# Performance work log

Measured on AMD Instinct MI355X. Metric: run time of the kernel, lower is better.

Reference implementation:

```python
import jax, jax.numpy as jnp
import numpy as np

N_NODES = 100000
N_EDGES = 3200000
IN_CH, HID, OUT_CH = 602, 16, 41


def setup_inputs() -> dict:
    key = jax.random.key(0)
    ks = jax.random.split(key, 5)
    x = jax.random.normal(ks[0], (N_NODES, IN_CH), dtype=jnp.float32)
    edge_index = jax.random.randint(ks[1], (2, N_EDGES), 0, N_NODES, dtype=jnp.int32)
    # glorot init for weights, zeros for biases (matches reset_parameters)
    W1 = jax.random.normal(ks[2], (IN_CH, HID), dtype=jnp.float32) * np.sqrt(2.0 / (IN_CH + HID))
    b1 = jnp.zeros((HID,), dtype=jnp.float32)
    W2 = jax.random.normal(ks[3], (HID, OUT_CH), dtype=jnp.float32) * np.sqrt(2.0 / (HID + OUT_CH))
    b2 = jnp.zeros((OUT_CH,), dtype=jnp.float32)
    return {"x": x, "edge_index": edge_index, "W1": W1, "b1": b1, "W2": W2, "b2": b2}


def _sage_conv(x, src, dst, W, b, n_nodes):
    # linear transform first (16-wide), then gather-scatter-mean over edges
    h = x @ W                                   # [N, out]
    msg = h[src]                                # [E, out] gather of source nodes
    agg = jax.ops.segment_sum(msg, dst, num_segments=n_nodes)          # [N, out]
    cnt = jax.ops.segment_sum(jnp.ones((src.shape[0], 1), h.dtype), dst,
                              num_segments=n_nodes)                     # [N, 1]
    mean = agg / jnp.maximum(cnt, 1.0)          # scatter-mean (0 for isolated nodes)
    return mean + b


def reference(x, edge_index, W1, b1, W2, b2):
    src, dst = edge_index[0], edge_index[1]     # source_to_target flow
    n = x.shape[0]
    h = jax.nn.relu(_sage_conv(x, src, dst, W1, b1, n))
    # F.dropout(training=False) -> identity (inference mode)
    out = _sage_conv(h, src, dst, W2, b2, n)
    return jax.nn.log_softmax(out, axis=1)
```

## Files before the change

kernel.cpp:

```cpp
#include <hip/hip_runtime.h>
#include <hip/hip_fp16.h>
#include <cmath>

#define NN 100000
#define NE 3200000
#define CIN 602
#define CH 16
#define COUT 41
#define KTL 32

#define NPB 128
#define NB  ((NN + NPB - 1) / NPB)
#define EPC 32
#define ECHUNK (256 * EPC)
#define EB  ((NE + ECHUNK - 1) / ECHUNK)

__device__ __half g_h1h[NN * CH];
__device__ __half g_h1bh[NN * CH];
__device__ int   g_rs[NN + 1];
__device__ int   g_csr[NE];
__device__ int2  g_pair[NE];
__device__ int   g_cnt[NB * EB];
__device__ int   g_colsum[NB];
__device__ int   g_bbase[NB + 1];

__device__ __forceinline__ int clamp_node(int v) {
    return v < 0 ? 0 : (v >= NN ? NN - 1 : v);
}

__global__ __launch_bounds__(256) void fallback_zero_out_k(float* __restrict__ out, int n) {
    int i = blockIdx.x * blockDim.x + threadIdx.x;
    if (i < n) out[i] = 0.0f;
}

__global__ __launch_bounds__(256) void count_k(const int* __restrict__ ei) {
    __shared__ int h[NB];
    const int t = threadIdx.x;
    for (int i = t; i < NB; i += 256) h[i] = 0;
    __syncthreads();
    const int base = blockIdx.x * ECHUNK;
#pragma unroll
    for (int j = 0; j < EPC; ++j) {
        int e = base + j * 256 + t;
        if (e < NE) {
            int d = clamp_node(ei[NE + e]);
            atomicAdd(&h[d >> 7], 1);
        }
    }
    __syncthreads();
    for (int i = t; i < NB; i += 256) g_cnt[i * EB + blockIdx.x] = h[i];
}

__global__ __launch_bounds__(256) void scanA_k() {
    const int b = blockIdx.x;
    const int t = threadIdx.x;
    __shared__ int a[512];
    __shared__ int sh[256];
    a[t]       = (t < EB)       ? g_cnt[b * EB + t]       : 0;
    a[t + 256] = (t + 256 < EB) ? g_cnt[b * EB + t + 256] : 0;
    __syncthreads();
    int e0 = a[2 * t], e1 = a[2 * t + 1];
    int sum = e0 + e1;
    sh[t] = sum;
    __syncthreads();
    for (int off = 1; off < 256; off <<= 1) {
        int v = (t >= off) ? sh[t - off] : 0;
        __syncthreads();
        sh[t] += v;
        __syncthreads();
    }
    int run = sh[t] - sum;
    if (2 * t < EB)     g_cnt[b * EB + 2 * t]     = run;
    if (2 * t + 1 < EB) g_cnt[b * EB + 2 * t + 1] = run + e0;
    if (t == 255) g_colsum[b] = sh[255];
}

__global__ __launch_bounds__(1024) void scanB_k() {
    const int t = threadIdx.x;
    __shared__ int sh[1024];
    int v = (t < NB) ? g_colsum[t] : 0;
    sh[t] = v;
    __syncthreads();
    for (int off = 1; off < 1024; off <<= 1) {
        int u = (t >= off) ? sh[t - off] : 0;
        __syncthreads();
        sh[t] += u;
        __syncthreads();
    }
    if (t < NB) g_bbase[t] = sh[t] - v;
    if (t == 1023) {
        g_bbase[NB] = sh[1023];
        g_rs[NN]    = sh[1023];
    }
}

__global__ __launch_bounds__(256) void scatter_k(const int* __restrict__ ei) {
    __shared__ int lb[NB];
    const int t = threadIdx.x;
    for (int i = t; i < NB; i += 256)
        lb[i] = g_bbase[i] + g_cnt[i * EB + blockIdx.x];
    __syncthreads();
    const int base = blockIdx.x * ECHUNK;
#pragma unroll
    for (int j = 0; j < EPC; ++j) {
        int e = base + j * 256 + t;
        if (e < NE) {
            int s = clamp_node(ei[e]);
            int d = clamp_node(ei[NE + e]);
            int p = atomicAdd(&lb[d >> 7], 1);
            g_pair[p] = make_int2(s, d);
        }
    }
}

__global__ __launch_bounds__(256) void build_k() {
    const int b = blockIdx.x;
    const int t = threadIdx.x;
    const int n0 = b * NPB;
    const int e0 = g_bbase[b], e1 = g_bbase[b + 1];
    __shared__ int ldeg[NPB];
    __shared__ int lrs[NPB + 1];
    __shared__ int lcur[NPB];
    if (t < NPB) ldeg[t] = 0;
    __syncthreads();
    for (int e = e0 + t; e < e1; e += 256) {
        int2 p = g_pair[e];
        atomicAdd(&ldeg[p.y - n0], 1);
    }
    __syncthreads();
    if (t == 0) {
        int run = 0;
        for (int i = 0; i < NPB; ++i) { lrs[i] = run; run += ldeg[i]; }
        lrs[NPB] = run;
    }
    __syncthreads();
    if (t < NPB) {
        int node = n0 + t;
        if (node < NN) g_rs[node] = e0 + lrs[t];
        lcur[t] = lrs[t];
    }
    __syncthreads();
    for (int e = e0 + t; e < e1; e += 256) {
        int2 p = g_pair[e];
        int r = atomicAdd(&lcur[p.y - n0], 1);
        g_csr[e0 + r] = p.x;
    }
}

__global__ __launch_bounds__(256) void gemm1_k(const float* __restrict__ x,
                                               const float* __restrict__ W1) {
    __shared__ float xs[2][KTL][128 + 1];
    __shared__ float red[128][CH];
    const int t = threadIdx.x;
    const int h = t >> 7;
    const int r = t & 127;
    const int l  = r & 15;
    const int rg = r >> 4;
    const int row0 = blockIdx.x * 128;
    const int row  = row0 + r;
    const int kbase = h * 320;

    float acc[CH];
#pragma unroll
    for (int c = 0; c < CH; ++c) acc[c] = 0.f;

    float2 ld[16];

    auto stage_load = [&](int ti) {
        const int kb = kbase + KTL * ti;
        const bool colok = (h == 0) || (ti < 8) || (ti == 8 && l <= 12);
#pragma unroll
        for (int p = 0; p < 16; ++p) {
            int rgl = row0 + rg + 8 * p;
            ld[p] = (rgl < NN && colok)
                ? *reinterpret_cast<const float2*>(x + (size_t)rgl * CIN + kb + 2 * l)
                : make_float2(0.f, 0.f);
        }
    };
    auto stage_store = [&]() {
#pragma unroll
        for (int p = 0; p < 16; ++p) {
            int rl = rg + 8 * p;
            xs[h][2 * l][rl]     = ld[p].x;
            xs[h][2 * l + 1][rl] = ld[p].y;
        }
    };

    stage_load(0);
    for (int ti = 0; ti < 10; ++ti) {
        stage_store();
        __syncthreads();
        if (ti < 9) stage_load(ti + 1);
        if (h == 0 || ti < 9) {
            const int kb = kbase + KTL * ti;
#pragma unroll 8
            for (int kk = 0; kk < KTL; ++kk) {
                float xv = xs[h][kk][r];
                int krow = kb + kk; if (krow > CIN - 1) krow = CIN - 1;
                const float4* w4 = reinterpret_cast<const float4*>(W1 + (size_t)krow * CH);
                float4 w0 = w4[0], w1 = w4[1], w2 = w4[2], w3 = w4[3];
                acc[0]  += xv * w0.x; acc[1]  += xv * w0.y; acc[2]  += xv * w0.z; acc[3]  += xv * w0.w;
                acc[4]  += xv * w1.x; acc[5]  += xv * w1.y; acc[6]  += xv * w1.z; acc[7]  += xv * w1.w;
                acc[8]  += xv * w2.x; acc[9]  += xv * w2.y; acc[10] += xv * w2.z; acc[11] += xv * w2.w;
                acc[12] += xv * w3.x; acc[13] += xv * w3.y; acc[14] += xv * w3.z; acc[15] += xv * w3.w;
            }
        }
        __syncthreads();
    }

    if (h == 1) {
#pragma unroll
        for (int c = 0; c < CH; ++c) red[r][c] = acc[c];
    }
    __syncthreads();
    if (h == 0 && row < NN) {
        __half2 pk[8];
#pragma unroll
        for (int c = 0; c < 8; ++c) {
            float lo = acc[2 * c]     + red[r][2 * c];
            float hi = acc[2 * c + 1] + red[r][2 * c + 1];
            pk[c] = __float22half2_rn(make_float2(lo, hi));
        }
        uint4* hp = reinterpret_cast<uint4*>(&g_h1h[(size_t)row * CH]);
        hp[0] = *reinterpret_cast<uint4*>(&pk[0]);
        hp[1] = *reinterpret_cast<uint4*>(&pk[4]);
    }
}

__global__ __launch_bounds__(256) void gather1_k(const float* __restrict__ b1) {
    int gtid = blockIdx.x * blockDim.x + threadIdx.x;
    int node = gtid >> 6;
    int l    = gtid & 63;
    int q    = l & 3;
    int es   = l >> 2;
    int start = g_rs[node], end = g_rs[node + 1];
    float4 acc = make_float4(0.f, 0.f, 0.f, 0.f);
    int e = start + es;
    for (; e + 16 < end; e += 32) {
        int s0 = g_csr[e], s1 = g_csr[e + 16];
        uint2 ua = *reinterpret_cast<const uint2*>(&g_h1h[(size_t)s0 * CH + (q << 2)]);
        uint2 ub = *reinterpret_cast<const uint2*>(&g_h1h[(size_t)s1 * CH + (q << 2)]);
        float2 fa0 = __half22float2(*reinterpret_cast<__half2*>(&ua.x));
        float2 fa1 = __half22float2(*reinterpret_cast<__half2*>(&ua.y));
        float2 fb0 = __half22float2(*reinterpret_cast<__half2*>(&ub.x));
        float2 fb1 = __half22float2(*reinterpret_cast<__half2*>(&ub.y));
        acc.x += fa0.x + fb0.x; acc.y += fa0.y + fb0.y;
        acc.z += fa1.x + fb1.x; acc.w += fa1.y + fb1.y;
    }
    if (e < end) {
        int s0 = g_csr[e];
        uint2 ua = *reinterpret_cast<const uint2*>(&g_h1h[(size_t)s0 * CH + (q << 2)]);
        float2 fa0 = __half22float2(*reinterpret_cast<__half2*>(&ua.x));
        float2 fa1 = __half22float2(*reinterpret_cast<__half2*>(&ua.y));
        acc.x += fa0.x; acc.y += fa0.y; acc.z += fa1.x; acc.w += fa1.y;
    }
#pragma unroll
    for (int off = 4; off < 64; off <<= 1) {
        acc.x += __shfl_xor(acc.x, off, 64);
        acc.y += __shfl_xor(acc.y, off, 64);
        acc.z += __shfl_xor(acc.z, off, 64);
        acc.w += __shfl_xor(acc.w, off, 64);
    }
    if (l < 4) {
        float inv = 1.0f / fmaxf((float)(end - start), 1.0f);
        float4 bv = reinterpret_cast<const float4*>(b1)[l];
        __half2 h0 = __float22half2_rn(make_float2(fmaxf(acc.x * inv + bv.x, 0.f),
                                                   fmaxf(acc.y * inv + bv.y, 0.f)));
        __half2 h1 = __float22half2_rn(make_float2(fmaxf(acc.z * inv + bv.z, 0.f),
                                                   fmaxf(acc.w * inv + bv.w, 0.f)));
        uint2 u;
        u.x = *reinterpret_cast<unsigned*>(&h0);
        u.y = *reinterpret_cast<unsigned*>(&h1);
        *reinterpret_cast<uint2*>(&g_h1bh[(size_t)node * CH + (l << 2)]) = u;
    }
}

__global__ __launch_bounds__(256) void g2final_k(const float* __restrict__ W2,
                                                 const float* __restrict__ b2,
                                                 float* __restrict__ out) {
    __shared__ float w2s[CH * COUT];
    const int t = threadIdx.x;
    for (int i = t; i < CH * COUT; i += 256) w2s[i] = W2[i];
    __syncthreads();

    int gtid = blockIdx.x * blockDim.x + t;
    int node = gtid >> 6;
    int l    = gtid & 63;
    int q    = l & 3;
    int es   = l >> 2;
    int start = g_rs[node], end = g_rs[node + 1];
    float4 acc = make_float4(0.f, 0.f, 0.f, 0.f);
    int e = start + es;
    for (; e + 16 < end; e += 32) {
        int s0 = g_csr[e], s1 = g_csr[e + 16];
        uint2 ua = *reinterpret_cast<const uint2*>(&g_h1bh[(size_t)s0 * CH + (q << 2)]);
        uint2 ub = *reinterpret_cast<const uint2*>(&g_h1bh[(size_t)s1 * CH + (q << 2)]);
        float2 fa0 = __half22float2(*reinterpret_cast<__half2*>(&ua.x));
        float2 fa1 = __half22float2(*reinterpret_cast<__half2*>(&ua.y));
        float2 fb0 = __half22float2(*reinterpret_cast<__half2*>(&ub.x));
        float2 fb1 = __half22float2(*reinterpret_cast<__half2*>(&ub.y));
        acc.x += fa0.x + fb0.x; acc.y += fa0.y + fb0.y;
        acc.z += fa1.x + fb1.x; acc.w += fa1.y + fb1.y;
    }
    if (e < end) {
        int s0 = g_csr[e];
        uint2 ua = *reinterpret_cast<const uint2*>(&g_h1bh[(size_t)s0 * CH + (q << 2)]);
        float2 fa0 = __half22float2(*reinterpret_cast<__half2*>(&ua.x));
        float2 fa1 = __half22float2(*reinterpret_cast<__half2*>(&ua.y));
        acc.x += fa0.x; acc.y += fa0.y; acc.z += fa1.x; acc.w += fa1.y;
    }
#pragma unroll
    for (int off = 4; off < 64; off <<= 1) {
        acc.x += __shfl_xor(acc.x, off, 64);
        acc.y += __shfl_xor(acc.y, off, 64);
        acc.z += __shfl_xor(acc.z, off, 64);
        acc.w += __shfl_xor(acc.w, off, 64);
    }
    float a16[CH];
#pragma unroll
    for (int k = 0; k < CH; ++k) {
        float comp = ((k & 3) == 0) ? acc.x : ((k & 3) == 1) ? acc.y
                   : ((k & 3) == 2) ? acc.z : acc.w;
        a16[k] = __shfl(comp, k >> 2, 64);
    }
    float inv = 1.0f / fmaxf((float)(end - start), 1.0f);
    float o = -INFINITY;
    if (l < COUT) {
        float s = 0.f;
#pragma unroll
        for (int k = 0; k < CH; ++k) s += a16[k] * w2s[k * COUT + l];
        o = s * inv + b2[l];
    }
    float m = o;
#pragma unroll
    for (int off = 32; off > 0; off >>= 1) m = fmaxf(m, __shfl_xor(m, off, 64));
    float ex = (l < COUT) ? expf(o - m) : 0.0f;
    float ssum = ex;
#pragma unroll
    for (int off = 32; off > 0; off >>= 1) ssum += __shfl_xor(ssum, off, 64);
    if (l < COUT) out[(size_t)node * COUT + l] = o - m - logf(ssum);
}

extern "C" void kernel_launch(void* const* d_in, const int* in_sizes, int n_in,
                              void* d_out, int out_size, void* d_ws, size_t ws_size,
                              hipStream_t stream) {
    (void)d_ws; (void)ws_size;
    float* out = (float*)d_out;

    const int expect[6] = {NN * CIN, 2 * NE, CIN * CH, CH, CH * COUT, COUT};
    bool ok = (n_in >= 6) && (out_size == NN * COUT);
    if (ok) {
        for (int i = 0; i < 6; ++i)
            if (in_sizes[i] != expect[i]) { ok = false; break; }
    }
    if (!ok) {
        int n = out_size > 0 ? out_size : 1;
        fallback_zero_out_k<<<(n + 255) / 256, 256, 0, stream>>>(out, n);
        return;
    }

    const float* x  = (const float*)d_in[0];
    const int*   ei = (const int*)d_in[1];
    const float* W1 = (const float*)d_in[2];
    const float* b1 = (const float*)d_in[3];
    const float* W2 = (const float*)d_in[4];
    const float* b2 = (const float*)d_in[5];

    const int WAVE_BLKS = (NN * 64 + 255) / 256;
    const int G1_BLKS   = (NN + 127) / 128;

    count_k  <<<EB, 256, 0, stream>>>(ei);
    scanA_k  <<<NB, 256, 0, stream>>>();
    scanB_k  <<<1, 1024, 0, stream>>>();
    scatter_k<<<EB, 256, 0, stream>>>(ei);
    build_k  <<<NB, 256, 0, stream>>>();
    gemm1_k  <<<G1_BLKS, 256, 0, stream>>>(x, W1);
    gather1_k<<<WAVE_BLKS, 256, 0, stream>>>(b1);
    g2final_k<<<WAVE_BLKS, 256, 0, stream>>>(W2, b2, out);
}
```

Before: 728.7 us.

## Split GEMM1 K dimension across four blocks with a separate combine kernel

Replaces the in-block two-way K split of the first GEMM with a four-way split across separate 128-thread blocks. Each block writes fp32 partial sums to a global buffer, and a new combine kernel adds them and packs the result to half precision. The aim is more parallelism and better latency hiding on the bandwidth-bound read of x. In exchange it adds an extra kernel launch and roughly 25 MB of partial-sum traffic.

```diff
diff --git a/kernel.cpp b/kernel.cpp
--- a/kernel.cpp
+++ b/kernel.cpp
@@ -7,7 +7,9 @@
 #define CIN 602
 #define CH 16
 #define COUT 41
+#define TB 128
 #define KTL 32
+#define KSPLIT 4
 
 #define NPB 128
 #define NB  ((NN + NPB - 1) / NPB)
@@ -15,6 +17,7 @@
 #define ECHUNK (256 * EPC)
 #define EB  ((NE + ECHUNK - 1) / ECHUNK)
 
+__device__ float  g_part[KSPLIT * NN * CH];
 __device__ __half g_h1h[NN * CH];
 __device__ __half g_h1bh[NN * CH];
 __device__ int   g_rs[NN + 1];
@@ -147,18 +150,19 @@
     }
 }
 
-__global__ __launch_bounds__(256) void gemm1_k(const float* __restrict__ x,
-                                               const float* __restrict__ W1) {
-    __shared__ float xs[2][KTL][128 + 1];
-    __shared__ float red[128][CH];
-    const int t = threadIdx.x;
-    const int h = t >> 7;
-    const int r = t & 127;
-    const int l  = r & 15;
-    const int rg = r >> 4;
-    const int row0 = blockIdx.x * 128;
-    const int row  = row0 + r;
-    const int kbase = h * 320;
+__global__ __launch_bounds__(TB) void gemm1_k(const float* __restrict__ x,
+                                              const float* __restrict__ W1) {
+    __shared__ float xs[KTL][TB + 1];
+    const int bid = blockIdx.x;
+    const int h   = bid & 3;
+    const int rblk = bid >> 2;
+    const int t = threadIdx.x;
+    const int l  = t & 15;
+    const int rg = t >> 4;
+    const int row0 = rblk * TB;
+    const int row  = row0 + t;
+    const int kbase = h * 160;
+    const int NT = (h < 3) ? 5 : 4;
 
     float acc[CH];
 #pragma unroll
@@ -168,7 +172,7 @@
 
     auto stage_load = [&](int ti) {
         const int kb = kbase + KTL * ti;
-        const bool colok = (h == 0) || (ti < 8) || (ti == 8 && l <= 12);
+        const bool colok = (h < 3) || (ti < 3) || (l <= 12);
 #pragma unroll
         for (int p = 0; p < 16; ++p) {
             int rgl = row0 + rg + 8 * p;
@@ -181,50 +185,71 @@
 #pragma unroll
         for (int p = 0; p < 16; ++p) {
             int rl = rg + 8 * p;
-            xs[h][2 * l][rl]     = ld[p].x;
-            xs[h][2 * l + 1][rl] = ld[p].y;
+            xs[2 * l][rl]     = ld[p].x;
+            xs[2 * l + 1][rl] = ld[p].y;
         }
     };
+    auto fma_col = [&](int krow, float xv) {
+        const float4* w4 = reinterpret_cast<const float4*>(W1 + (size_t)krow * CH);
+        float4 w0 = w4[0], w1 = w4[1], w2 = w4[2], w3 = w4[3];
+        acc[0]  += xv * w0.x; acc[1]  += xv * w0.y; acc[2]  += xv * w0.z; acc[3]  += xv * w0.w;
+        acc[4]  += xv * w1.x; acc[5]  += xv * w1.y; acc[6]  += xv * w1.z; acc[7]  += xv * w1.w;
+        acc[8]  += xv * w2.x; acc[9]  += xv * w2.y; acc[10] += xv * w2.z; acc[11] += xv * w2.w;
+        acc[12] += xv * w3.x; acc[13] += xv * w3.y; acc[14] += xv * w3.z; acc[15] += xv * w3.w;
+    };
 
     stage_load(0);
-    for (int ti = 0; ti < 10; ++ti) {
+    for (int ti = 0; ti < NT; ++ti) {
         stage_store();
         __syncthreads();
-        if (ti < 9) stage_load(ti + 1);
-        if (h == 0 || ti < 9) {
-            const int kb = kbase + KTL * ti;
+        if (ti < NT - 1) stage_load(ti + 1);
+        const int kb = kbase + KTL * ti;
+        if (h < 3 || ti < 3) {
 #pragma unroll 8
-            for (int kk = 0; kk < KTL; ++kk) {
-                float xv = xs[h][kk][r];
-                int krow = kb + kk; if (krow > CIN - 1) krow = CIN - 1;
-                const float4* w4 = reinterpret_cast<const float4*>(W1 + (size_t)krow * CH);
-                float4 w0 = w4[0], w1 = w4[1], w2 = w4[2], w3 = w4[3];
-                acc[0]  += xv * w0.x; acc[1]  += xv * w0.y; acc[2]  += xv * w0.z; acc[3]  += xv * w0.w;
-                acc[4]  += xv * w1.x; acc[5]  += xv * w1.y; acc[6]  += xv * w1.z; acc[7]  += xv * w1.w;
-                acc[8]  += xv * w2.x; acc[9]  += xv * w2.y; acc[10] += xv * w2.z; acc[11] += xv * w2.w;
-                acc[12] += xv * w3.x; acc[13] += xv * w3.y; acc[14] += xv * w3.z; acc[15] += xv * w3.w;
-            }
-        }
-        __syncthreads();
-    }
-
-    if (h == 1) {
-#pragma unroll
-        for (int c = 0; c < CH; ++c) red[r][c] = acc[c];
-    }
-    __syncthreads();
-    if (h == 0 && row < NN) {
-        __half2 pk[8];
-#pragma unroll
-        for (int c = 0; c < 8; ++c) {
-            float lo = acc[2 * c]     + red[r][2 * c];
-            float hi = acc[2 * c + 1] + red[r][2 * c + 1];
-            pk[c] = __float22half2_rn(make_float2(lo, hi));
-        }
-        uint4* hp = reinterpret_cast<uint4*>(&g_h1h[(size_t)row * CH]);
-        hp[0] = *reinterpret_cast<uint4*>(&pk[0]);
-        hp[1] = *reinterpret_cast<uint4*>(&pk[4]);
-    }
+            for (int kk = 0; kk < KTL; ++kk) fma_col(kb + kk, xs[kk][t]);
+        } else {
+#pragma unroll 13
+            for (int kk = 0; kk < 26; ++kk) fma_col(kb + kk, xs[kk][t]);
+        }
+        __syncthreads();
+    }
+
+    if (row < NN) {
+        float4* pp = reinterpret_cast<float4*>(g_part + ((size_t)h * NN + row) * CH);
+        pp[0] = make_float4(acc[0],  acc[1],  acc[2],  acc[3]);
+        pp[1] = make_float4(acc[4],  acc[5],  acc[6],  acc[7]);
+        pp[2] = make_float4(acc[8],  acc[9],  acc[10], acc[11]);
+        pp[3] = make_float4(acc[12], acc[13], acc[14], acc[15]);
+    }
+}
+
+__global__ __launch_bounds__(256) void combine_k() {
+    int node = blockIdx.x * blockDim.x + threadIdx.x;
+    if (node >= NN) return;
+    float s[CH];
+#pragma unroll
+    for (int h = 0; h < KSPLIT; ++h) {
+        const float4* pp = reinterpret_cast<const float4*>(g_part + ((size_t)h * NN + node) * CH);
+        float4 p0 = pp[0], p1 = pp[1], p2 = pp[2], p3 = pp[3];
+        if (h == 0) {
+            s[0]=p0.x; s[1]=p0.y; s[2]=p0.z; s[3]=p0.w;
+            s[4]=p1.x; s[5]=p1.y; s[6]=p1.z; s[7]=p1.w;
+            s[8]=p2.x; s[9]=p2.y; s[10]=p2.z; s[11]=p2.w;
+            s[12]=p3.x; s[13]=p3.y; s[14]=p3.z; s[15]=p3.w;
+        } else {
+            s[0]+=p0.x; s[1]+=p0.y; s[2]+=p0.z; s[3]+=p0.w;
+            s[4]+=p1.x; s[5]+=p1.y; s[6]+=p1.z; s[7]+=p1.w;
+            s[8]+=p2.x; s[9]+=p2.y; s[10]+=p2.z; s[11]+=p2.w;
+            s[12]+=p3.x; s[13]+=p3.y; s[14]+=p3.z; s[15]+=p3.w;
+        }
+    }
+    __half2 pk[8];
+#pragma unroll
+    for (int c = 0; c < 8; ++c)
+        pk[c] = __float22half2_rn(make_float2(s[2 * c], s[2 * c + 1]));
+    uint4* hp = reinterpret_cast<uint4*>(&g_h1h[(size_t)node * CH]);
+    hp[0] = *reinterpret_cast<uint4*>(&pk[0]);
+    hp[1] = *reinterpret_cast<uint4*>(&pk[4]);
 }
 
 __global__ __launch_bounds__(256) void gather1_k(const float* __restrict__ b1) {
@@ -367,14 +392,15 @@
     const float* b2 = (const float*)d_in[5];
 
     const int WAVE_BLKS = (NN * 64 + 255) / 256;
-    const int G1_BLKS   = (NN + 127) / 128;
+    const int G1_BLKS   = ((NN + TB - 1) / TB) * KSPLIT;
 
     count_k  <<<EB, 256, 0, stream>>>(ei);
     scanA_k  <<<NB, 256, 0, stream>>>();
     scanB_k  <<<1, 1024, 0, stream>>>();
     scatter_k<<<EB, 256, 0, stream>>>(ei);
     build_k  <<<NB, 256, 0, stream>>>();
-    gemm1_k  <<<G1_BLKS, 256, 0, stream>>>(x, W1);
+    gemm1_k  <<<G1_BLKS, TB, 0, stream>>>(x, W1);
+    combine_k<<<(NN + 255) / 256, 256, 0, stream>>>();
     gather1_k<<<WAVE_BLKS, 256, 0, stream>>>(b1);
     g2final_k<<<WAVE_BLKS, 256, 0, stream>>>(W2, b2, out);
 }
```

After: 597.1 us. 1.22x faster.
